# Kernel tuning notes

Measured on AMD Instinct MI355X. Metric: run time of the kernel, lower is better.

Reference implementation:

```python
import jax, jax.numpy as jnp
import numpy as np

N_USERS = 50000
N_ITEMS = 50000
N = N_USERS + N_ITEMS
DIM = 64
N_LAYERS = 3
N_EDGES = 1250000
BN_EPS = 1e-5


def setup_inputs() -> dict:
    key = jax.random.key(0)
    k_x, k_e, k_w, k_b = jax.random.split(key, 4)
    x = jax.random.normal(k_x, (N, DIM), dtype=jnp.float32)
    edge_index = jax.random.randint(k_e, (2, N_EDGES), 0, N, dtype=jnp.int64)
    # Glorot-ish init for the per-layer GCNConv linear weights [L, DIM, DIM]
    Ws = jax.random.normal(k_w, (N_LAYERS, DIM, DIM), dtype=jnp.float32) * (1.0 / np.sqrt(DIM))
    bs = jnp.zeros((N_LAYERS, DIM), dtype=jnp.float32)
    gamma = jnp.ones((DIM,), dtype=jnp.float32)
    beta = jnp.zeros((DIM,), dtype=jnp.float32)
    return {"x": x, "edge_index": edge_index, "Ws": Ws, "bs": bs,
            "gamma": gamma, "beta": beta}


def _gcn_conv(x, W, b, src, dst, deg_inv_sqrt):
    # PyG GCNConv: h = x @ W^T ; out_i = sum_{j->i} norm_ji * h_j + b
    h = x @ W.T                                   # [N, DIM]
    norm = deg_inv_sqrt[src] * deg_inv_sqrt[dst]  # [E2]
    msg = h[src] * norm[:, None]                  # gather over irregular edges
    out = jax.ops.segment_sum(msg, dst, num_segments=N)
    return out + b


def reference(x, edge_index, Ws, bs, gamma, beta):
    # Add self-loops once (same augmented graph for every layer).
    loops = jnp.arange(N, dtype=edge_index.dtype)
    src = jnp.concatenate([edge_index[0], loops])  # source nodes j
    dst = jnp.concatenate([edge_index[1], loops])  # target nodes i
    # Symmetric normalization degrees (edge weight 1, counted at targets).
    deg = jax.ops.segment_sum(jnp.ones_like(dst, dtype=x.dtype), dst, num_segments=N)
    deg_inv_sqrt = jnp.where(deg > 0, jax.lax.rsqrt(deg), 0.0)

    for i in range(N_LAYERS):
        x = _gcn_conv(x, Ws[i], bs[i], src, dst, deg_inv_sqrt)

    # BatchNorm1d (training-mode batch statistics, biased variance)
    mean = jnp.mean(x, axis=0)
    var = jnp.mean((x - mean) ** 2, axis=0)
    x = (x - mean) * jax.lax.rsqrt(var + BN_EPS) * gamma + beta

    users, items = x[:N_USERS], x[N_USERS:]
    return users, items
```

## Files before the change

### kernel.cpp

```cpp
#include <hip/hip_runtime.h>

#define NN      100000
#define NUSERS  50000
#define NE      1250000
#define DIM     64
#define BN_EPS  1e-5f
#define NBUCK   8
#define NCHUNK  256
#define SLOT    40
#define CPAD    8

typedef __attribute__((ext_vector_type(8))) short s16x8;
typedef __attribute__((ext_vector_type(4))) float f32x4;

__device__ __forceinline__ short f2b(float f) {
    unsigned u = __builtin_bit_cast(unsigned, f);
    u = (u + 0x7fffu + ((u >> 16) & 1u)) >> 16;
    return (short)u;
}
__device__ __forceinline__ float b2f(unsigned short s) {
    unsigned u = ((unsigned)s) << 16;
    return __builtin_bit_cast(float, u);
}

__global__ __launch_bounds__(256) void place_part(const int* __restrict__ ei,
                                                  int* __restrict__ cursor,
                                                  int* __restrict__ csr_src) {
    int lane = threadIdx.x & 63, wave = threadIdx.x >> 6;
    int B = blockIdx.x & (NBUCK - 1);
    int gw = (blockIdx.x >> 3) * 4 + wave;
    const int NW = NCHUNK * 4;
    int gwr = gw + B * (NW / NBUCK);
    if (gwr >= NW) gwr -= NW;
    const int per = (NE + NW - 1) / NW;
    int e0 = gwr * per;
    int e1 = e0 + per; if (e1 > NE) e1 = NE;
    for (int eb = e0; eb < e1; eb += 8 * 64) {
        int d[8], s[8];
        bool k[8];
#pragma unroll
        for (int u = 0; u < 8; ++u) {
            int ee = eb + u * 64 + lane;
            bool in = ee < e1;
            int idx = in ? ee : e0;
            d[u] = ei[NE + idx];
            s[u] = ei[idx];
            k[u] = in && ((d[u] / 12500) == B);
        }
#pragma unroll
        for (int u = 0; u < 8; ++u) {
            if (k[u]) {
                int pos = atomicAdd(&cursor[d[u] * CPAD], 1);
                if (pos < SLOT) csr_src[d[u] * SLOT + pos] = s[u];
            }
        }
    }
}

__global__ __launch_bounds__(256) void dinv_c0(const int* __restrict__ cursor,
                                               float* __restrict__ dinv,
                                               const float* __restrict__ Ws,
                                               const float* __restrict__ bs,
                                               float* __restrict__ c0) {
    int v = blockIdx.x * blockDim.x + threadIdx.x;
    if (v < NN) dinv[v] = rsqrtf((float)cursor[v * CPAD] + 1.0f);
    if (v < 128) {
        int l = v >> 6, j = v & 63;
        const float* Wl = Ws + (size_t)(l + 1) * 4096;
        const float* bl = bs + l * 64;
        float s = 0.0f;
        for (int k = 0; k < 64; ++k) s += bl[k] * Wl[j * 64 + k];
        c0[v] = s;
    }
}

__global__ __launch_bounds__(256) void gemm_l0(const float* __restrict__ Xin,
                                               const float* __restrict__ W,
                                               const float* __restrict__ dinv,
                                               unsigned short* __restrict__ Gb) {
    __shared__ s16x8 WL[8][64];
    int lane = threadIdx.x & 63;
    int n16 = lane & 15, quad = lane >> 4;

#pragma unroll
    for (int e = threadIdx.x; e < 512; e += 256) {
        int ln = e & 63, tc = e >> 6;
        int tt = tc >> 1, cc = tc & 1;
        int m16 = ln & 15, qq = ln >> 4;
        const float4* wp = (const float4*)(W + (tt * 16 + m16) * 64 + cc * 32 + qq * 8);
        float4 w0 = wp[0], w1 = wp[1];
        s16x8 f;
        f[0] = f2b(w0.x); f[1] = f2b(w0.y); f[2] = f2b(w0.z); f[3] = f2b(w0.w);
        f[4] = f2b(w1.x); f[5] = f2b(w1.y); f[6] = f2b(w1.z); f[7] = f2b(w1.w);
        WL[tc][ln] = f;
    }
    __syncthreads();

    s16x8 bfrag[4][2];
#pragma unroll
    for (int t = 0; t < 4; ++t)
#pragma unroll
        for (int c = 0; c < 2; ++c)
            bfrag[t][c] = WL[t * 2 + c][lane];

    int wid = (blockIdx.x * blockDim.x + threadIdx.x) >> 6;
    int nw  = (gridDim.x * blockDim.x) >> 6;
    for (int tile = wid; tile < NN / 16; tile += nw) {
        int r0 = tile * 16;
        int m  = r0 + n16;
        s16x8 a[2];
#pragma unroll
        for (int c = 0; c < 2; ++c) {
            const float4* xp = (const float4*)(Xin + (size_t)m * 64 + c * 32 + quad * 8);
            float4 x0 = xp[0], x1 = xp[1];
            s16x8 f;
            f[0] = f2b(x0.x); f[1] = f2b(x0.y); f[2] = f2b(x0.z); f[3] = f2b(x0.w);
            f[4] = f2b(x1.x); f[5] = f2b(x1.y); f[6] = f2b(x1.z); f[7] = f2b(x1.w);
            a[c] = f;
        }
        f32x4 acc[4] = {{0,0,0,0},{0,0,0,0},{0,0,0,0},{0,0,0,0}};
#pragma unroll
        for (int c = 0; c < 2; ++c)
#pragma unroll
            for (int t = 0; t < 4; ++t)
                acc[t] = __builtin_amdgcn_mfma_f32_16x16x32_bf16(a[c], bfrag[t][c], acc[t], 0, 0, 0);

        float dvr[4];
#pragma unroll
        for (int r = 0; r < 4; ++r) dvr[r] = dinv[r0 + quad * 4 + r];
#pragma unroll
        for (int t = 0; t < 4; ++t)
#pragma unroll
            for (int r = 0; r < 4; ++r)
                Gb[(size_t)(r0 + quad * 4 + r) * 64 + t * 16 + n16] =
                    (unsigned short)f2b(dvr[r] * acc[t][r]);
    }
}

template <int BASE>
__device__ __forceinline__ void gbatch8(const unsigned short* __restrict__ Gb,
                                        int v, int c, int g, int n, int ir,
                                        float& ax, float& ay, float& az, float& aw) {
    ushort4 val[8];
    float msk[8];
#pragma unroll
    for (int u = 0; u < 8; ++u) {
        int j = BASE + u;
        int s = __shfl(ir, g * 16 + (j & 15), 64);
        bool ok = j < n;
        msk[u] = ok ? 1.0f : 0.0f;
        val[u] = *(const ushort4*)(Gb + (size_t)(ok ? s : v) * 64 + c * 4);
    }
#pragma unroll
    for (int u = 0; u < 8; ++u) {
        ax = fmaf(msk[u], b2f(val[u].x), ax);
        ay = fmaf(msk[u], b2f(val[u].y), ay);
        az = fmaf(msk[u], b2f(val[u].z), az);
        aw = fmaf(msk[u], b2f(val[u].w), aw);
    }
}

template <int FUSE>
__global__ __launch_bounds__(256) void gather_fused(const int* __restrict__ cursor,
                                                    const int* __restrict__ csr_src,
                                                    const unsigned short* __restrict__ Gb_in,
                                                    const float* __restrict__ W,
                                                    const float* __restrict__ dinv,
                                                    const float* __restrict__ c0,
                                                    unsigned short* __restrict__ outp) {
    __shared__ s16x8 WL[8][64];
    __shared__ float AT[16][68];
    int lane = threadIdx.x & 63, wave = threadIdx.x >> 6;
    int c = lane & 15, g = lane >> 4;

    if (FUSE) {
#pragma unroll
        for (int e = threadIdx.x; e < 512; e += 256) {
            int ln = e & 63, tc = e >> 6;
            int tt = tc >> 1, cc2 = tc & 1;
            int m16 = ln & 15, qq = ln >> 4;
            const float4* wp = (const float4*)(W + (tt * 16 + m16) * 64 + cc2 * 32 + qq * 8);
            float4 w0 = wp[0], w1 = wp[1];
            s16x8 f;
            f[0] = f2b(w0.x); f[1] = f2b(w0.y); f[2] = f2b(w0.z); f[3] = f2b(w0.w);
            f[4] = f2b(w1.x); f[5] = f2b(w1.y); f[6] = f2b(w1.z); f[7] = f2b(w1.w);
            WL[tc][ln] = f;
        }
    }

    int r0 = blockIdx.x * 16;
    int v  = r0 + wave * 4 + g;
    int n = cursor[v * CPAD]; if (n > SLOT) n = SLOT;
    int i0 = csr_src[v * SLOT + c];
    ushort4 sv = *(const ushort4*)(Gb_in + (size_t)v * 64 + c * 4);
    float ax = b2f(sv.x), ay = b2f(sv.y), az = b2f(sv.z), aw = b2f(sv.w);
    if (n > 0)  gbatch8<0 >(Gb_in, v, c, g, n, i0, ax, ay, az, aw);
    if (n > 8)  gbatch8<8 >(Gb_in, v, c, g, n, i0, ax, ay, az, aw);
    if (n > 16) {
        int i1 = csr_src[v * SLOT + 16 + c];
        gbatch8<16>(Gb_in, v, c, g, n, i1, ax, ay, az, aw);
        if (n > 24) gbatch8<24>(Gb_in, v, c, g, n, i1, ax, ay, az, aw);
        if (n > 32) {
            int i2 = csr_src[v * SLOT + 32 + (c & 7)];
            gbatch8<32>(Gb_in, v, c, g, n, i2, ax, ay, az, aw);
        }
    }

    if (!FUSE) {
        ushort4 o;
        o.x = (unsigned short)f2b(ax); o.y = (unsigned short)f2b(ay);
        o.z = (unsigned short)f2b(az); o.w = (unsigned short)f2b(aw);
        *(ushort4*)(outp + (size_t)v * 64 + c * 4) = o;
        return;
    }

    float4 f4; f4.x = ax; f4.y = ay; f4.z = az; f4.w = aw;
    *(float4*)&AT[wave * 4 + g][c * 4] = f4;
    __syncthreads();
    if (wave != 0) return;

    int n16 = lane & 15, quad = lane >> 4;
    s16x8 a[2];
#pragma unroll
    for (int cc2 = 0; cc2 < 2; ++cc2) {
        const float* ap = &AT[n16][cc2 * 32 + quad * 8];
        s16x8 f;
#pragma unroll
        for (int q2 = 0; q2 < 8; ++q2) f[q2] = f2b(ap[q2]);
        a[cc2] = f;
    }
    s16x8 bfrag[4][2];
#pragma unroll
    for (int t = 0; t < 4; ++t)
#pragma unroll
        for (int cc2 = 0; cc2 < 2; ++cc2)
            bfrag[t][cc2] = WL[t * 2 + cc2][lane];

    f32x4 acc[4] = {{0,0,0,0},{0,0,0,0},{0,0,0,0},{0,0,0,0}};
#pragma unroll
    for (int cc2 = 0; cc2 < 2; ++cc2)
#pragma unroll
        for (int t = 0; t < 4; ++t)
            acc[t] = __builtin_amdgcn_mfma_f32_16x16x32_bf16(a[cc2], bfrag[t][cc2], acc[t], 0, 0, 0);

    float dvr[4];
#pragma unroll
    for (int r = 0; r < 4; ++r) dvr[r] = dinv[r0 + quad * 4 + r];
#pragma unroll
    for (int t = 0; t < 4; ++t) {
        float cc2 = c0[t * 16 + n16];
#pragma unroll
        for (int r = 0; r < 4; ++r) {
            float dv = dvr[r];
            float g2 = dv * dv * acc[t][r] + dv * cc2;
            outp[(size_t)(r0 + quad * 4 + r) * 64 + t * 16 + n16] = (unsigned short)f2b(g2);
        }
    }
}

__global__ __launch_bounds__(256) void bn_stats(const unsigned short* __restrict__ ACCb,
                                                const float* __restrict__ dinv,
                                                const float* __restrict__ blast,
                                                float* __restrict__ sums) {
    int j = threadIdx.x & 63;
    float b = blast[j];
    int wid = (blockIdx.x * blockDim.x + threadIdx.x) >> 6;
    int nw  = (gridDim.x * blockDim.x) >> 6;
    float s = 0.0f, s2 = 0.0f;
    for (int v = wid; v < NN; v += nw) {
        float y = dinv[v] * b2f(ACCb[(size_t)v * 64 + j]) + b;
        s += y;
        s2 += y * y;
    }
    __shared__ float ls[256], ls2[256];
    ls[threadIdx.x] = s;
    ls2[threadIdx.x] = s2;
    __syncthreads();
    if (threadIdx.x < 64) {
        s  = ls[threadIdx.x] + ls[threadIdx.x + 64] + ls[threadIdx.x + 128] + ls[threadIdx.x + 192];
        s2 = ls2[threadIdx.x] + ls2[threadIdx.x + 64] + ls2[threadIdx.x + 128] + ls2[threadIdx.x + 192];
        atomicAdd(&sums[j], s);
        atomicAdd(&sums[64 + j], s2);
    }
}

__global__ __launch_bounds__(256) void bn_apply(const unsigned short* __restrict__ ACCb,
                                                const float* __restrict__ dinv,
                                                const float* __restrict__ blast,
                                                const float* __restrict__ sums,
                                                const float* __restrict__ gamma,
                                                const float* __restrict__ beta,
                                                float* __restrict__ out) {
    const float invN = 1.0f / (float)NN;
    int stride = gridDim.x * blockDim.x;
    for (int i = blockIdx.x * blockDim.x + threadIdx.x; i < NN * 64; i += stride) {
        int j = i & 63;
        int v = i >> 6;
        float mean = sums[j] * invN;
        float var  = sums[64 + j] * invN - mean * mean;
        float y = dinv[v] * b2f(ACCb[i]) + blast[j];
        out[i] = (y - mean) * rsqrtf(var + BN_EPS) * gamma[j] + beta[j];
    }
}

extern "C" void kernel_launch(void* const* d_in, const int* in_sizes, int n_in,
                              void* d_out, int out_size, void* d_ws, size_t ws_size,
                              hipStream_t stream) {
    const float* x     = (const float*)d_in[0];
    const int*   ei    = (const int*)d_in[1];
    const float* Ws    = (const float*)d_in[2];
    const float* bs    = (const float*)d_in[3];
    const float* gamma = (const float*)d_in[4];
    const float* beta  = (const float*)d_in[5];
    float* out = (float*)d_out;

    char* ws = (char*)d_ws;
    size_t off = 0;
    unsigned short* ACCb = (unsigned short*)(ws + off); off += (size_t)NN * 64 * 2;
    unsigned short* GbA  = (unsigned short*)(ws + off); off += (size_t)NN * 64 * 2;
    unsigned short* GbB  = (unsigned short*)(ws + off); off += (size_t)NN * 64 * 2;
    float* dinv    = (float*)(ws + off); off += (size_t)NN * 4;
    float* sums    = (float*)(ws + off); off += 128 * 4;
    float* c0      = (float*)(ws + off); off += 128 * 4;
    int*   cursor  = (int*)(ws + off);   off += (size_t)NN * CPAD * 4;
    int*   csr_src = (int*)(ws + off);   off += (size_t)NN * SLOT * 4;

    hipMemsetAsync(cursor, 0, (size_t)NN * CPAD * sizeof(int), stream);
    hipMemsetAsync(sums, 0, 128 * sizeof(float), stream);

    place_part<<<NBUCK * NCHUNK, 256, 0, stream>>>(ei, cursor, csr_src);
    dinv_c0<<<(NN + 255) / 256, 256, 0, stream>>>(cursor, dinv, Ws, bs, c0);

    gemm_l0<<<1563, 256, 0, stream>>>(x, Ws, dinv, GbA);
    gather_fused<1><<<6250, 256, 0, stream>>>(cursor, csr_src, GbA,
                                              Ws + 4096, dinv, c0, GbB);
    gather_fused<1><<<6250, 256, 0, stream>>>(cursor, csr_src, GbB,
                                              Ws + 8192, dinv, c0 + 64, GbA);
    gather_fused<0><<<6250, 256, 0, stream>>>(cursor, csr_src, GbA,
                                              nullptr, nullptr, nullptr, ACCb);

    bn_stats<<<2048, 256, 0, stream>>>(ACCb, dinv, bs + 128, sums);
    bn_apply<<<2048, 256, 0, stream>>>(ACCb, dinv, bs + 128, sums, gamma, beta, out);
}
```

Baseline: 316.1 us.

## Fuse BN statistics into final gather and use nontemporal edge loads

The last gather kernel now applies the per-node dinv scale and final bias, stores the finished value, and reduces per-column sum and sum-of-squares via wave shuffles and shared memory, then does atomic adds. This removes the separate bn_stats pass over the 12.8MB bf16 buffer and simplifies bn_apply. Edge-index loads in the partition kernel become nontemporal. The cost is 128 extra atomics per block across 6250 blocks, and statistics are now computed on fp32 values before bf16 rounding, which changes numerics slightly.

```diff
diff --git a/kernel.cpp b/kernel.cpp
--- a/kernel.cpp
+++ b/kernel.cpp
@@ -43,8 +43,8 @@
             int ee = eb + u * 64 + lane;
             bool in = ee < e1;
             int idx = in ? ee : e0;
-            d[u] = ei[NE + idx];
-            s[u] = ei[idx];
+            d[u] = __builtin_nontemporal_load(&ei[NE + idx]);
+            s[u] = __builtin_nontemporal_load(&ei[idx]);
             k[u] = in && ((d[u] / 12500) == B);
         }
 #pragma unroll
@@ -167,7 +167,8 @@
                                                     const float* __restrict__ W,
                                                     const float* __restrict__ dinv,
                                                     const float* __restrict__ c0,
-                                                    unsigned short* __restrict__ outp) {
+                                                    unsigned short* __restrict__ outp,
+                                                    float* __restrict__ sums) {
     __shared__ s16x8 WL[8][64];
     __shared__ float AT[16][68];
     int lane = threadIdx.x & 63, wave = threadIdx.x >> 6;
@@ -207,10 +208,34 @@
     }
 
     if (!FUSE) {
+        float dv = dinv[v];
+        float y0 = dv * ax + c0[c * 4 + 0];
+        float y1 = dv * ay + c0[c * 4 + 1];
+        float y2 = dv * az + c0[c * 4 + 2];
+        float y3 = dv * aw + c0[c * 4 + 3];
         ushort4 o;
-        o.x = (unsigned short)f2b(ax); o.y = (unsigned short)f2b(ay);
-        o.z = (unsigned short)f2b(az); o.w = (unsigned short)f2b(aw);
+        o.x = (unsigned short)f2b(y0); o.y = (unsigned short)f2b(y1);
+        o.z = (unsigned short)f2b(y2); o.w = (unsigned short)f2b(y3);
         *(ushort4*)(outp + (size_t)v * 64 + c * 4) = o;
+        float s0 = y0, s1 = y1, s2 = y2, s3 = y3;
+        float q0 = y0 * y0, q1 = y1 * y1, q2 = y2 * y2, q3 = y3 * y3;
+#pragma unroll
+        for (int off = 16; off < 64; off <<= 1) {
+            s0 += __shfl_xor(s0, off, 64); s1 += __shfl_xor(s1, off, 64);
+            s2 += __shfl_xor(s2, off, 64); s3 += __shfl_xor(s3, off, 64);
+            q0 += __shfl_xor(q0, off, 64); q1 += __shfl_xor(q1, off, 64);
+            q2 += __shfl_xor(q2, off, 64); q3 += __shfl_xor(q3, off, 64);
+        }
+        if (g == 0) {
+            *(float4*)&AT[wave * 2][c * 4]     = make_float4(s0, s1, s2, s3);
+            *(float4*)&AT[wave * 2 + 1][c * 4] = make_float4(q0, q1, q2, q3);
+        }
+        __syncthreads();
+        if (threadIdx.x < 128) {
+            int j = threadIdx.x & 63, kind = threadIdx.x >> 6;
+            float t = AT[0 + kind][j] + AT[2 + kind][j] + AT[4 + kind][j] + AT[6 + kind][j];
+            atomicAdd(&sums[kind * 64 + j], t);
+        }
         return;
     }
 
@@ -258,35 +283,7 @@
     }
 }
 
-__global__ __launch_bounds__(256) void bn_stats(const unsigned short* __restrict__ ACCb,
-                                                const float* __restrict__ dinv,
-                                                const float* __restrict__ blast,
-                                                float* __restrict__ sums) {
-    int j = threadIdx.x & 63;
-    float b = blast[j];
-    int wid = (blockIdx.x * blockDim.x + threadIdx.x) >> 6;
-    int nw  = (gridDim.x * blockDim.x) >> 6;
-    float s = 0.0f, s2 = 0.0f;
-    for (int v = wid; v < NN; v += nw) {
-        float y = dinv[v] * b2f(ACCb[(size_t)v * 64 + j]) + b;
-        s += y;
-        s2 += y * y;
-    }
-    __shared__ float ls[256], ls2[256];
-    ls[threadIdx.x] = s;
-    ls2[threadIdx.x] = s2;
-    __syncthreads();
-    if (threadIdx.x < 64) {
-        s  = ls[threadIdx.x] + ls[threadIdx.x + 64] + ls[threadIdx.x + 128] + ls[threadIdx.x + 192];
-        s2 = ls2[threadIdx.x] + ls2[threadIdx.x + 64] + ls2[threadIdx.x + 128] + ls2[threadIdx.x + 192];
-        atomicAdd(&sums[j], s);
-        atomicAdd(&sums[64 + j], s2);
-    }
-}
-
 __global__ __launch_bounds__(256) void bn_apply(const unsigned short* __restrict__ ACCb,
-                                                const float* __restrict__ dinv,
-                                                const float* __restrict__ blast,
                                                 const float* __restrict__ sums,
                                                 const float* __restrict__ gamma,
                                                 const float* __restrict__ beta,
@@ -295,10 +292,9 @@
     int stride = gridDim.x * blockDim.x;
     for (int i = blockIdx.x * blockDim.x + threadIdx.x; i < NN * 64; i += stride) {
         int j = i & 63;
-        int v = i >> 6;
         float mean = sums[j] * invN;
         float var  = sums[64 + j] * invN - mean * mean;
-        float y = dinv[v] * b2f(ACCb[i]) + blast[j];
+        float y = b2f(ACCb[i]);
         out[i] = (y - mean) * rsqrtf(var + BN_EPS) * gamma[j] + beta[j];
     }
 }
@@ -333,12 +329,11 @@
 
     gemm_l0<<<1563, 256, 0, stream>>>(x, Ws, dinv, GbA);
     gather_fused<1><<<6250, 256, 0, stream>>>(cursor, csr_src, GbA,
-                                              Ws + 4096, dinv, c0, GbB);
+                                              Ws + 4096, dinv, c0, GbB, nullptr);
     gather_fused<1><<<6250, 256, 0, stream>>>(cursor, csr_src, GbB,
-                                              Ws + 8192, dinv, c0 + 64, GbA);
+                                              Ws + 8192, dinv, c0 + 64, GbA, nullptr);
     gather_fused<0><<<6250, 256, 0, stream>>>(cursor, csr_src, GbA,
-                                              nullptr, nullptr, nullptr, ACCb);
-
-    bn_stats<<<2048, 256, 0, stream>>>(ACCb, dinv, bs + 128, sums);
-    bn_apply<<<2048, 256, 0, stream>>>(ACCb, dinv, bs + 128, sums, gamma, beta, out);
-}
+                                              nullptr, dinv, bs + 128, ACCb, sums);
+
+    bn_apply<<<2048, 256, 0, stream>>>(ACCb, sums, gamma, beta, out);
+}
```

Measured after the change: 401.2 us. 1.27x slower.

## Overlap edge placement with layer-0 GEMM in one launch; scale by dinv afterwards

Applied to the files above, without the earlier changes.

Merges the CSR edge-placement pass and the layer-0 GEMM into a single kernel whose blocks are split by role, so the atomic-bound placement and the compute-bound GEMM can run at the same time. Because dinv isn't known until placement finishes, the GEMM writes unscaled bf16 output. A new finish_pass kernel computes dinv, rescales the GEMM output in place and computes c0. This removes one launch and one serial stage, but adds an extra read and write of the bf16 buffer and a second bf16 rounding.

```diff
diff --git a/kernel.cpp b/kernel.cpp
--- a/kernel.cpp
+++ b/kernel.cpp
@@ -23,65 +23,50 @@
     return __builtin_bit_cast(float, u);
 }
 
-__global__ __launch_bounds__(256) void place_part(const int* __restrict__ ei,
+__global__ __launch_bounds__(256) void place_gemm(const int* __restrict__ ei,
                                                   int* __restrict__ cursor,
-                                                  int* __restrict__ csr_src) {
+                                                  int* __restrict__ csr_src,
+                                                  const float* __restrict__ x,
+                                                  const float* __restrict__ W,
+                                                  unsigned short* __restrict__ Gb) {
+    __shared__ s16x8 WL[8][64];
     int lane = threadIdx.x & 63, wave = threadIdx.x >> 6;
-    int B = blockIdx.x & (NBUCK - 1);
-    int gw = (blockIdx.x >> 3) * 4 + wave;
-    const int NW = NCHUNK * 4;
-    int gwr = gw + B * (NW / NBUCK);
-    if (gwr >= NW) gwr -= NW;
-    const int per = (NE + NW - 1) / NW;
-    int e0 = gwr * per;
-    int e1 = e0 + per; if (e1 > NE) e1 = NE;
-    for (int eb = e0; eb < e1; eb += 8 * 64) {
-        int d[8], s[8];
-        bool k[8];
-#pragma unroll
-        for (int u = 0; u < 8; ++u) {
-            int ee = eb + u * 64 + lane;
-            bool in = ee < e1;
-            int idx = in ? ee : e0;
-            d[u] = ei[NE + idx];
-            s[u] = ei[idx];
-            k[u] = in && ((d[u] / 12500) == B);
-        }
-#pragma unroll
-        for (int u = 0; u < 8; ++u) {
-            if (k[u]) {
-                int pos = atomicAdd(&cursor[d[u] * CPAD], 1);
-                if (pos < SLOT) csr_src[d[u] * SLOT + pos] = s[u];
+    int role = (blockIdx.x >> 3) & 1;
+    int ci = ((blockIdx.x >> 4) << 3) | (blockIdx.x & 7);
+
+    if (role == 0) {
+        int B = ci & (NBUCK - 1);
+        int gw = (ci >> 3) * 4 + wave;
+        const int NW = NCHUNK * 4;
+        int gwr = gw + B * (NW / NBUCK);
+        if (gwr >= NW) gwr -= NW;
+        const int per = (NE + NW - 1) / NW;
+        int e0 = gwr * per;
+        int e1 = e0 + per; if (e1 > NE) e1 = NE;
+        for (int eb = e0; eb < e1; eb += 8 * 64) {
+            int d[8], s[8];
+            bool k[8];
+#pragma unroll
+            for (int u = 0; u < 8; ++u) {
+                int ee = eb + u * 64 + lane;
+                bool in = ee < e1;
+                int idx = in ? ee : e0;
+                d[u] = ei[NE + idx];
+                s[u] = ei[idx];
+                k[u] = in && ((d[u] / 12500) == B);
+            }
+#pragma unroll
+            for (int u = 0; u < 8; ++u) {
+                if (k[u]) {
+                    int pos = atomicAdd(&cursor[d[u] * CPAD], 1);
+                    if (pos < SLOT) csr_src[d[u] * SLOT + pos] = s[u];
+                }
             }
         }
-    }
-}
-
-__global__ __launch_bounds__(256) void dinv_c0(const int* __restrict__ cursor,
-                                               float* __restrict__ dinv,
-                                               const float* __restrict__ Ws,
-                                               const float* __restrict__ bs,
-                                               float* __restrict__ c0) {
-    int v = blockIdx.x * blockDim.x + threadIdx.x;
-    if (v < NN) dinv[v] = rsqrtf((float)cursor[v * CPAD] + 1.0f);
-    if (v < 128) {
-        int l = v >> 6, j = v & 63;
-        const float* Wl = Ws + (size_t)(l + 1) * 4096;
-        const float* bl = bs + l * 64;
-        float s = 0.0f;
-        for (int k = 0; k < 64; ++k) s += bl[k] * Wl[j * 64 + k];
-        c0[v] = s;
-    }
-}
-
-__global__ __launch_bounds__(256) void gemm_l0(const float* __restrict__ Xin,
-                                               const float* __restrict__ W,
-                                               const float* __restrict__ dinv,
-                                               unsigned short* __restrict__ Gb) {
-    __shared__ s16x8 WL[8][64];
-    int lane = threadIdx.x & 63;
+        return;
+    }
+
     int n16 = lane & 15, quad = lane >> 4;
-
 #pragma unroll
     for (int e = threadIdx.x; e < 512; e += 256) {
         int ln = e & 63, tc = e >> 6;
@@ -96,6 +81,8 @@
     }
     __syncthreads();
 
+    int tile = ci * 4 + wave;
+    if (tile >= NN / 16) return;
     s16x8 bfrag[4][2];
 #pragma unroll
     for (int t = 0; t < 4; ++t)
@@ -103,37 +90,56 @@
         for (int c = 0; c < 2; ++c)
             bfrag[t][c] = WL[t * 2 + c][lane];
 
-    int wid = (blockIdx.x * blockDim.x + threadIdx.x) >> 6;
-    int nw  = (gridDim.x * blockDim.x) >> 6;
-    for (int tile = wid; tile < NN / 16; tile += nw) {
-        int r0 = tile * 16;
-        int m  = r0 + n16;
-        s16x8 a[2];
-#pragma unroll
-        for (int c = 0; c < 2; ++c) {
-            const float4* xp = (const float4*)(Xin + (size_t)m * 64 + c * 32 + quad * 8);
-            float4 x0 = xp[0], x1 = xp[1];
-            s16x8 f;
-            f[0] = f2b(x0.x); f[1] = f2b(x0.y); f[2] = f2b(x0.z); f[3] = f2b(x0.w);
-            f[4] = f2b(x1.x); f[5] = f2b(x1.y); f[6] = f2b(x1.z); f[7] = f2b(x1.w);
-            a[c] = f;
-        }
-        f32x4 acc[4] = {{0,0,0,0},{0,0,0,0},{0,0,0,0},{0,0,0,0}};
-#pragma unroll
-        for (int c = 0; c < 2; ++c)
-#pragma unroll
-            for (int t = 0; t < 4; ++t)
-                acc[t] = __builtin_amdgcn_mfma_f32_16x16x32_bf16(a[c], bfrag[t][c], acc[t], 0, 0, 0);
-
-        float dvr[4];
-#pragma unroll
-        for (int r = 0; r < 4; ++r) dvr[r] = dinv[r0 + quad * 4 + r];
+    int r0 = tile * 16;
+    int m  = r0 + n16;
+    s16x8 a[2];
+#pragma unroll
+    for (int c = 0; c < 2; ++c) {
+        const float4* xp = (const float4*)(x + (size_t)m * 64 + c * 32 + quad * 8);
+        float4 x0 = xp[0], x1 = xp[1];
+        s16x8 f;
+        f[0] = f2b(x0.x); f[1] = f2b(x0.y); f[2] = f2b(x0.z); f[3] = f2b(x0.w);
+        f[4] = f2b(x1.x); f[5] = f2b(x1.y); f[6] = f2b(x1.z); f[7] = f2b(x1.w);
+        a[c] = f;
+    }
+    f32x4 acc[4] = {{0,0,0,0},{0,0,0,0},{0,0,0,0},{0,0,0,0}};
+#pragma unroll
+    for (int c = 0; c < 2; ++c)
 #pragma unroll
         for (int t = 0; t < 4; ++t)
-#pragma unroll
-            for (int r = 0; r < 4; ++r)
-                Gb[(size_t)(r0 + quad * 4 + r) * 64 + t * 16 + n16] =
-                    (unsigned short)f2b(dvr[r] * acc[t][r]);
+            acc[t] = __builtin_amdgcn_mfma_f32_16x16x32_bf16(a[c], bfrag[t][c], acc[t], 0, 0, 0);
+#pragma unroll
+    for (int t = 0; t < 4; ++t)
+#pragma unroll
+        for (int r = 0; r < 4; ++r)
+            Gb[(size_t)(r0 + quad * 4 + r) * 64 + t * 16 + n16] =
+                (unsigned short)f2b(acc[t][r]);
+}
+
+__global__ __launch_bounds__(256) void finish_pass(const int* __restrict__ cursor,
+                                                   float* __restrict__ dinv,
+                                                   const float* __restrict__ Ws,
+                                                   const float* __restrict__ bs,
+                                                   float* __restrict__ c0,
+                                                   unsigned short* __restrict__ Gb) {
+    int idx = blockIdx.x * 256 + threadIdx.x;
+    int v = idx >> 4, c = idx & 15;
+    float dv = rsqrtf((float)cursor[v * CPAD] + 1.0f);
+    if (c == 0) dinv[v] = dv;
+    ushort4 t = *(const ushort4*)(Gb + (size_t)v * 64 + c * 4);
+    ushort4 o;
+    o.x = (unsigned short)f2b(dv * b2f(t.x));
+    o.y = (unsigned short)f2b(dv * b2f(t.y));
+    o.z = (unsigned short)f2b(dv * b2f(t.z));
+    o.w = (unsigned short)f2b(dv * b2f(t.w));
+    *(ushort4*)(Gb + (size_t)v * 64 + c * 4) = o;
+    if (blockIdx.x == 0 && threadIdx.x < 128) {
+        int l = threadIdx.x >> 6, j = threadIdx.x & 63;
+        const float* Wl = Ws + (size_t)(l + 1) * 4096;
+        const float* bl = bs + l * 64;
+        float s = 0.0f;
+        for (int k = 0; k < 64; ++k) s += bl[k] * Wl[j * 64 + k];
+        c0[threadIdx.x] = s;
     }
 }
 
@@ -328,10 +334,9 @@
     hipMemsetAsync(cursor, 0, (size_t)NN * CPAD * sizeof(int), stream);
     hipMemsetAsync(sums, 0, 128 * sizeof(float), stream);
 
-    place_part<<<NBUCK * NCHUNK, 256, 0, stream>>>(ei, cursor, csr_src);
-    dinv_c0<<<(NN + 255) / 256, 256, 0, stream>>>(cursor, dinv, Ws, bs, c0);
-
-    gemm_l0<<<1563, 256, 0, stream>>>(x, Ws, dinv, GbA);
+    place_gemm<<<4096, 256, 0, stream>>>(ei, cursor, csr_src, x, Ws, GbA);
+    finish_pass<<<NN / 16, 256, 0, stream>>>(cursor, dinv, Ws, bs, c0, GbA);
+
     gather_fused<1><<<6250, 256, 0, stream>>>(cursor, csr_src, GbA,
                                               Ws + 4096, dinv, c0, GbB);
     gather_fused<1><<<6250, 256, 0, stream>>>(cursor, csr_src, GbB,
```

Result: slower. 326.1 us (+3.2%).
